# Kernel optimization log

Measured on AMD Instinct MI355X. Metric: run time of the kernel, lower is better.

The kernel has to match this reference:

```python
import jax, jax.numpy as jnp
import numpy as np

B, N, E, H = 2, 2048, 1024, 16
D = E // H  # head_dim = 64


def setup_inputs() -> dict:
    key = jax.random.key(0)
    ks = jax.random.split(key, 8)
    s = 1.0 / np.sqrt(D)
    return {
        "query": jax.random.normal(ks[0], (B, N, E), jnp.float32),
        "key": jax.random.normal(ks[1], (B, N, E), jnp.float32),
        "value": jax.random.normal(ks[2], (B, N, E), jnp.float32),
        "mask": jax.random.randint(ks[3], (B, N), 0, 2, jnp.int32),
        # per-head Linear weights, torch layout (out_features, in_features) stacked over heads
        "Wq": jax.random.uniform(ks[4], (H, D, D), jnp.float32, -s, s),
        "Wk": jax.random.uniform(ks[5], (H, D, D), jnp.float32, -s, s),
        "Wv": jax.random.uniform(ks[6], (H, D, D), jnp.float32, -s, s),
        "Wo": jax.random.uniform(ks[7], (E, E), jnp.float32, -1.0 / np.sqrt(E), 1.0 / np.sqrt(E)),
    }


def reference(query, key, value, mask, Wq, Wk, Wv, Wo):
    b, n, e = query.shape
    h, d, _ = Wq.shape
    q = query.reshape(b, n, h, d)
    k = key.reshape(b, n, h, d)
    v = value.reshape(b, n, h, d)
    # per-head Linear (no bias): x @ W[i].T, batched over heads
    qh = jnp.einsum('bnhd,hed->bnhe', q, Wq)
    kh = jnp.einsum('bnhd,hed->bnhe', k, Wk)
    vh = jnp.einsum('bnhd,hed->bnhe', v, Wv)
    # NOTE: original scales by sqrt(embed_size), not sqrt(head_dim)
    scores = jnp.einsum('bqhd,bkhd->bhqk', qh, kh) / (e ** 0.5)
    # NOTE: mask is unsqueezed on the KEY axis position in torch (dim=2),
    # so it masks entire QUERY rows, broadcasting over keys.
    scores = jnp.where(mask[:, None, :, None] == 0, jnp.float32(-1e28), scores)
    probs = jax.nn.softmax(scores, axis=-1)
    attn = jnp.einsum('bhqk,bkhd->bqhd', probs, vh).reshape(b, n, e)
    return attn @ Wo.T
```

## Files before the change

### kernel.cpp

```cpp
#include <hip/hip_runtime.h>
#include <hip/hip_bf16.h>

#define B_ 2
#define N_ 2048
#define E_ 1024
#define H_ 16
#define D_ 64
#define BH_ (B_ * H_)

typedef __attribute__((ext_vector_type(4))) float f32x4;
typedef __attribute__((ext_vector_type(8))) short bf16x8;
typedef __attribute__((ext_vector_type(4))) short s16x4;
typedef __attribute__((ext_vector_type(4))) int i32x4;

#define MFMA(a, b, c) __builtin_amdgcn_mfma_f32_16x16x32_bf16(a, b, c, 0, 0, 0)

static __device__ __forceinline__ unsigned short f2bf(float f) {
    unsigned int u = __builtin_bit_cast(unsigned int, f);
    u += 0x7fff + ((u >> 16) & 1);
    return (unsigned short)(u >> 16);
}
static __device__ __forceinline__ float bf2f(unsigned short s) {
    unsigned int u = ((unsigned int)s) << 16;
    return __builtin_bit_cast(float, u);
}
static __device__ __forceinline__ int pack2bf(float lo, float hi) {
    return (int)f2bf(lo) | ((int)f2bf(hi) << 16);
}
static __device__ __forceinline__ bf16x8 cvt8(const float* __restrict__ p) {
    f32x4 a = *(const f32x4*)p;
    f32x4 b = *(const f32x4*)(p + 4);
    bf16x8 r;
    r[0] = (short)f2bf(a.x); r[1] = (short)f2bf(a.y);
    r[2] = (short)f2bf(a.z); r[3] = (short)f2bf(a.w);
    r[4] = (short)f2bf(b.x); r[5] = (short)f2bf(b.y);
    r[6] = (short)f2bf(b.z); r[7] = (short)f2bf(b.w);
    return r;
}

__global__ __launch_bounds__(256, 4)
void proj_kernel(const float* __restrict__ q, const float* __restrict__ k,
                 const float* __restrict__ v,
                 const float* __restrict__ Wq, const float* __restrict__ Wk,
                 const float* __restrict__ Wv,
                 unsigned short* __restrict__ qh, unsigned short* __restrict__ kh,
                 unsigned short* __restrict__ vt) {
    const int z = blockIdx.z;
    const float* X = (z == 0) ? q : (z == 1) ? k : v;
    const float* W = (z == 0) ? Wq : (z == 1) ? Wk : Wv;
    unsigned short* out = (z == 0) ? qh : (z == 1) ? kh : vt;

    const int lane = threadIdx.x & 63;
    const int wave = threadIdx.x >> 6;
    const int l16  = lane & 15;
    const int quad = lane >> 4;
    const int bh = blockIdx.y;
    const int b = bh >> 4, h = bh & 15;
    const int n0 = blockIdx.x * 64;

    const int tok = n0 + wave * 16 + l16;
    const float* xrow = X + ((size_t)(b * N_ + tok)) * E_ + h * 64;
    bf16x8 xf[2];
    xf[0] = cvt8(xrow + quad * 8);
    xf[1] = cvt8(xrow + 32 + quad * 8);

    const float* Wh = W + (size_t)h * 64 * 64;
    bf16x8 wf[4][2];
#pragma unroll
    for (int t4 = 0; t4 < 4; ++t4) {
        const float* wrow = Wh + (t4 * 16 + l16) * 64;
        wf[t4][0] = cvt8(wrow + quad * 8);
        wf[t4][1] = cvt8(wrow + 32 + quad * 8);
    }

    if (z != 2) {
#pragma unroll
        for (int t4 = 0; t4 < 4; ++t4) {
            f32x4 a = {0.f, 0.f, 0.f, 0.f};
            a = MFMA(xf[0], wf[t4][0], a);
            a = MFMA(xf[1], wf[t4][1], a);
#pragma unroll
            for (int r = 0; r < 4; ++r) {
                int tk = n0 + wave * 16 + quad * 4 + r;
                out[((size_t)bh * N_ + tk) * 64 + t4 * 16 + l16] = (unsigned short)f2bf(a[r]);
            }
        }
    } else {
#pragma unroll
        for (int mi = 0; mi < 4; ++mi) {
            f32x4 a = {0.f, 0.f, 0.f, 0.f};
            a = MFMA(wf[mi][0], xf[0], a);
            a = MFMA(wf[mi][1], xf[1], a);
#pragma unroll
            for (int r = 0; r < 4; ++r) {
                int dout = mi * 16 + quad * 4 + r;
                out[((size_t)bh * 64 + dout) * N_ + (n0 + wave * 16 + l16)] =
                    (unsigned short)f2bf(a[r]);
            }
        }
    }
}

__global__ __launch_bounds__(256)
void cvt_wo_kernel(const float* __restrict__ wo, unsigned short* __restrict__ wob) {
    int idx = blockIdx.x * 256 + threadIdx.x;
    f32x4 v = *(const f32x4*)(wo + (size_t)idx * 4);
    s16x4 r = {(short)f2bf(v.x), (short)f2bf(v.y), (short)f2bf(v.z), (short)f2bf(v.w)};
    *(s16x4*)(wob + (size_t)idx * 4) = r;
}

__global__ __launch_bounds__(256, 2)
void attn_kernel(const unsigned short* __restrict__ qh,
                 const unsigned short* __restrict__ kh,
                 const unsigned short* __restrict__ vt,
                 const int* __restrict__ mask,
                 unsigned short* __restrict__ attnb) {
    __shared__ short Kb[2][64][72];
    __shared__ short Vb[2][64][72];

    const int tid  = threadIdx.x;
    const int lane = tid & 63;
    const int wave = tid >> 6;
    const int l16  = lane & 15;
    const int quad = lane >> 4;

    const int flat = blockIdx.y * gridDim.x + blockIdx.x;
    const int qblk = flat >> 5;
    const int rem  = flat & 31;
    const int bh   = ((rem & 7) << 2) | (rem >> 3);
    const int b = bh >> 4, h = bh & 15;
    const int q0 = qblk * 128 + wave * 32;

    const unsigned short* kbase = kh + (size_t)bh * N_ * 64;
    const unsigned short* vbase = vt + (size_t)bh * 64 * N_;

    const int c0i = tid;
    const int c1i = tid + 256;

    const int srcA = (((quad * 2) & 3) << 4) + l16;
    const int srcB = (((quad * 2 + 1) & 3) << 4) + l16;
    const bool hiSel = (quad >= 2);

    const float qscale = 1.44269504f * 0.03125f;
    bf16x8 qf[2][2];
#pragma unroll
    for (int qi = 0; qi < 2; ++qi) {
        const int qrow_idx = q0 + qi * 16 + l16;
        const int mk = mask[b * N_ + qrow_idx];
        const unsigned short* qrow = qh + ((size_t)bh * N_ + qrow_idx) * 64;
#pragma unroll
        for (int c = 0; c < 2; ++c) {
            bf16x8 raw = *(const bf16x8*)(qrow + c * 32 + quad * 8);
            bf16x8 t;
#pragma unroll
            for (int j = 0; j < 8; ++j) {
                float f = bf2f((unsigned short)raw[j]) * qscale;
                t[j] = mk ? (short)f2bf(f) : (short)0;
            }
            qf[qi][c] = t;
        }
    }

    float lI[2] = {0.f, 0.f};
    f32x4 o[4][2];
#pragma unroll
    for (int mi = 0; mi < 4; ++mi)
#pragma unroll
        for (int qi = 0; qi < 2; ++qi) o[mi][qi] = (f32x4){0.f, 0.f, 0.f, 0.f};

    bf16x8 gK0, gK1, gV0, gV1;
    gK0 = *(const bf16x8*)(kbase + c0i * 8);
    gK1 = *(const bf16x8*)(kbase + c1i * 8);
    gV0 = *(const bf16x8*)(vbase + (size_t)(c0i >> 3) * N_ + (c0i & 7) * 8);
    gV1 = *(const bf16x8*)(vbase + (size_t)(c1i >> 3) * N_ + (c1i & 7) * 8);
    *(bf16x8*)(&Kb[0][c0i >> 3][(c0i & 7) * 8]) = gK0;
    *(bf16x8*)(&Kb[0][c1i >> 3][(c1i & 7) * 8]) = gK1;
    *(bf16x8*)(&Vb[0][c0i >> 3][(c0i & 7) * 8]) = gV0;
    *(bf16x8*)(&Vb[0][c1i >> 3][(c1i & 7) * 8]) = gV1;
    __syncthreads();

    for (int kt = 0; kt < N_ / 64; ++kt) {
        const int cur = kt & 1;

        if (kt + 1 < N_ / 64) {
            const int k0n = (kt + 1) * 64;
            gK0 = *(const bf16x8*)(kbase + (size_t)k0n * 64 + c0i * 8);
            gK1 = *(const bf16x8*)(kbase + (size_t)k0n * 64 + c1i * 8);
            gV0 = *(const bf16x8*)(vbase + (size_t)(c0i >> 3) * N_ + k0n + (c0i & 7) * 8);
            gV1 = *(const bf16x8*)(vbase + (size_t)(c1i >> 3) * N_ + k0n + (c1i & 7) * 8);
        }

        bf16x8 ka[4][2];
#pragma unroll
        for (int t4 = 0; t4 < 4; ++t4) {
            ka[t4][0] = *(const bf16x8*)(&Kb[cur][t4 * 16 + l16][quad * 8]);
            ka[t4][1] = *(const bf16x8*)(&Kb[cur][t4 * 16 + l16][32 + quad * 8]);
        }

        f32x4 s[2][4];
#pragma unroll
        for (int qi = 0; qi < 2; ++qi)
#pragma unroll
            for (int t4 = 0; t4 < 4; ++t4) {
                f32x4 z = {0.f, 0.f, 0.f, 0.f};
                z = MFMA(ka[t4][0], qf[qi][0], z);
                z = MFMA(ka[t4][1], qf[qi][1], z);
                s[qi][t4] = z;
            }

        bf16x8 va[4][2];
#pragma unroll
        for (int mi = 0; mi < 4; ++mi) {
            va[mi][0] = *(const bf16x8*)(&Vb[cur][mi * 16 + l16][quad * 8]);
            va[mi][1] = *(const bf16x8*)(&Vb[cur][mi * 16 + l16][32 + quad * 8]);
        }

#pragma unroll
        for (int qi = 0; qi < 2; ++qi) {
            float rsum = 0.f;
            int pk[4][2];
#pragma unroll
            for (int t4 = 0; t4 < 4; ++t4) {
                f32x4 p;
#pragma unroll
                for (int r = 0; r < 4; ++r) {
                    p[r] = __builtin_amdgcn_exp2f(s[qi][t4][r]);
                    rsum += p[r];
                }
                pk[t4][0] = pack2bf(p.x, p.y);
                pk[t4][1] = pack2bf(p.z, p.w);
            }
            rsum += __shfl_xor(rsum, 16);
            rsum += __shfl_xor(rsum, 32);
            lI[qi] += rsum;

            i32x4 w0, w1;
#pragma unroll
            for (int d = 0; d < 2; ++d) {
                int a0 = __shfl(pk[0][d], srcA), a1 = __shfl(pk[1][d], srcA);
                int b0 = __shfl(pk[0][d], srcB), b1 = __shfl(pk[1][d], srcB);
                w0[d]     = hiSel ? a1 : a0;
                w0[2 + d] = hiSel ? b1 : b0;
                int c0 = __shfl(pk[2][d], srcA), c1 = __shfl(pk[3][d], srcA);
                int e0 = __shfl(pk[2][d], srcB), e1 = __shfl(pk[3][d], srcB);
                w1[d]     = hiSel ? c1 : c0;
                w1[2 + d] = hiSel ? e1 : e0;
            }
            bf16x8 pb0 = __builtin_bit_cast(bf16x8, w0);
            bf16x8 pb1 = __builtin_bit_cast(bf16x8, w1);

#pragma unroll
            for (int mi = 0; mi < 4; ++mi) {
                o[mi][qi] = MFMA(va[mi][0], pb0, o[mi][qi]);
                o[mi][qi] = MFMA(va[mi][1], pb1, o[mi][qi]);
            }
        }

        if (kt + 1 < N_ / 64) {
            const int nxt = cur ^ 1;
            *(bf16x8*)(&Kb[nxt][c0i >> 3][(c0i & 7) * 8]) = gK0;
            *(bf16x8*)(&Kb[nxt][c1i >> 3][(c1i & 7) * 8]) = gK1;
            *(bf16x8*)(&Vb[nxt][c0i >> 3][(c0i & 7) * 8]) = gV0;
            *(bf16x8*)(&Vb[nxt][c1i >> 3][(c1i & 7) * 8]) = gV1;
            __syncthreads();
        }
    }

#pragma unroll
    for (int qi = 0; qi < 2; ++qi) {
        const float inv = 1.0f / lI[qi];
        const int qrow_idx = q0 + qi * 16 + l16;
#pragma unroll
        for (int mi = 0; mi < 4; ++mi) {
            f32x4 ov = o[mi][qi];
            s16x4 pkk = {(short)f2bf(ov.x * inv), (short)f2bf(ov.y * inv),
                         (short)f2bf(ov.z * inv), (short)f2bf(ov.w * inv)};
            int d0 = mi * 16 + quad * 4;
            *(s16x4*)(attnb + ((size_t)(b * N_ + qrow_idx)) * E_ + h * 64 + d0) = pkk;
        }
    }
}

__global__ __launch_bounds__(256, 4)
void out_gemm_kernel(const unsigned short* __restrict__ attnb,
                     const unsigned short* __restrict__ wob,
                     float* __restrict__ out) {
    const int lane = threadIdx.x & 63;
    const int wave = threadIdx.x >> 6;
    const int l16  = lane & 15;
    const int quad = lane >> 4;

    const int flat = blockIdx.y * gridDim.x + blockIdx.x;
    const int t0b  = ((flat & 7) << 2) | ((flat >> 3) & 3);
    const int c0b  = flat >> 5;
    const int t0 = t0b * 128 + wave * 32;
    const int c0 = c0b * 64;

    f32x4 acc[2][4];
#pragma unroll
    for (int mi = 0; mi < 2; ++mi)
#pragma unroll
        for (int t4 = 0; t4 < 4; ++t4) acc[mi][t4] = (f32x4){0.f, 0.f, 0.f, 0.f};

#pragma unroll 2
    for (int kc = 0; kc < E_ / 32; ++kc) {
        bf16x8 a[2], bb[4];
#pragma unroll
        for (int mi = 0; mi < 2; ++mi)
            a[mi] = *(const bf16x8*)(attnb + (size_t)(t0 + mi * 16 + l16) * E_ +
                                     kc * 32 + quad * 8);
#pragma unroll
        for (int t4 = 0; t4 < 4; ++t4)
            bb[t4] = *(const bf16x8*)(wob + (size_t)(c0 + t4 * 16 + l16) * E_ +
                                      kc * 32 + quad * 8);
#pragma unroll
        for (int mi = 0; mi < 2; ++mi)
#pragma unroll
            for (int t4 = 0; t4 < 4; ++t4)
                acc[mi][t4] = MFMA(a[mi], bb[t4], acc[mi][t4]);
    }

#pragma unroll
    for (int mi = 0; mi < 2; ++mi)
#pragma unroll
        for (int t4 = 0; t4 < 4; ++t4)
#pragma unroll
            for (int r = 0; r < 4; ++r)
                out[(size_t)(t0 + mi * 16 + quad * 4 + r) * E_ + c0 + t4 * 16 + l16] =
                    acc[mi][t4][r];
}

extern "C" void kernel_launch(void* const* d_in, const int* in_sizes, int n_in,
                              void* d_out, int out_size, void* d_ws, size_t ws_size,
                              hipStream_t stream) {
    const float* q    = (const float*)d_in[0];
    const float* k    = (const float*)d_in[1];
    const float* v    = (const float*)d_in[2];
    const int*   mask = (const int*)d_in[3];
    const float* Wq   = (const float*)d_in[4];
    const float* Wk   = (const float*)d_in[5];
    const float* Wv   = (const float*)d_in[6];
    const float* Wo   = (const float*)d_in[7];
    float* out = (float*)d_out;

    char* ws = (char*)d_ws;
    unsigned short* qh    = (unsigned short*)(ws);
    unsigned short* kh    = (unsigned short*)(ws + (size_t)8 * 1024 * 1024);
    unsigned short* vt    = (unsigned short*)(ws + (size_t)16 * 1024 * 1024);
    unsigned short* attnb = (unsigned short*)(ws + (size_t)24 * 1024 * 1024);
    unsigned short* wob   = (unsigned short*)(ws);

    dim3 blk(256);
    proj_kernel<<<dim3(N_ / 64, BH_, 3), blk, 0, stream>>>(q, k, v, Wq, Wk, Wv, qh, kh, vt);
    attn_kernel<<<dim3(16, 32), blk, 0, stream>>>(qh, kh, vt, mask, attnb);
    cvt_wo_kernel<<<dim3(E_ * E_ / 1024), blk, 0, stream>>>(Wo, wob);
    out_gemm_kernel<<<dim3(32, 16), blk, 0, stream>>>(attnb, wob, out);
}
```

Measured before the change: 241.8 us.

## Fold Q scale and mask into projection; LDS-tiled out GEMM with async loads

Result: faster. 224.2 us (-7.3%).

```diff
diff --git a/kernel.cpp b/kernel.cpp
--- a/kernel.cpp
+++ b/kernel.cpp
@@ -15,6 +15,9 @@
 
 #define MFMA(a, b, c) __builtin_amdgcn_mfma_f32_16x16x32_bf16(a, b, c, 0, 0, 0)
 
+#define AS1(p) ((const __attribute__((address_space(1))) unsigned int*)(p))
+#define AS3(p) ((__attribute__((address_space(3))) unsigned int*)(p))
+
 static __device__ __forceinline__ unsigned short f2bf(float f) {
     unsigned int u = __builtin_bit_cast(unsigned int, f);
     u += 0x7fff + ((u >> 16) & 1);
@@ -27,14 +30,14 @@
 static __device__ __forceinline__ int pack2bf(float lo, float hi) {
     return (int)f2bf(lo) | ((int)f2bf(hi) << 16);
 }
-static __device__ __forceinline__ bf16x8 cvt8(const float* __restrict__ p) {
+static __device__ __forceinline__ bf16x8 cvt8s(const float* __restrict__ p, float sc) {
     f32x4 a = *(const f32x4*)p;
     f32x4 b = *(const f32x4*)(p + 4);
     bf16x8 r;
-    r[0] = (short)f2bf(a.x); r[1] = (short)f2bf(a.y);
-    r[2] = (short)f2bf(a.z); r[3] = (short)f2bf(a.w);
-    r[4] = (short)f2bf(b.x); r[5] = (short)f2bf(b.y);
-    r[6] = (short)f2bf(b.z); r[7] = (short)f2bf(b.w);
+    r[0] = (short)f2bf(a.x * sc); r[1] = (short)f2bf(a.y * sc);
+    r[2] = (short)f2bf(a.z * sc); r[3] = (short)f2bf(a.w * sc);
+    r[4] = (short)f2bf(b.x * sc); r[5] = (short)f2bf(b.y * sc);
+    r[6] = (short)f2bf(b.z * sc); r[7] = (short)f2bf(b.w * sc);
     return r;
 }
 
@@ -43,12 +46,14 @@
                  const float* __restrict__ v,
                  const float* __restrict__ Wq, const float* __restrict__ Wk,
                  const float* __restrict__ Wv,
+                 const int* __restrict__ mask,
                  unsigned short* __restrict__ qh, unsigned short* __restrict__ kh,
                  unsigned short* __restrict__ vt) {
     const int z = blockIdx.z;
     const float* X = (z == 0) ? q : (z == 1) ? k : v;
     const float* W = (z == 0) ? Wq : (z == 1) ? Wk : Wv;
     unsigned short* out = (z == 0) ? qh : (z == 1) ? kh : vt;
+    const float wscale = (z == 0) ? (1.44269504f * 0.03125f) : 1.0f;
 
     const int lane = threadIdx.x & 63;
     const int wave = threadIdx.x >> 6;
@@ -57,45 +62,39 @@
     const int bh = blockIdx.y;
     const int b = bh >> 4, h = bh & 15;
     const int n0 = blockIdx.x * 64;
-
     const int tok = n0 + wave * 16 + l16;
+
     const float* xrow = X + ((size_t)(b * N_ + tok)) * E_ + h * 64;
     bf16x8 xf[2];
-    xf[0] = cvt8(xrow + quad * 8);
-    xf[1] = cvt8(xrow + 32 + quad * 8);
+    xf[0] = cvt8s(xrow + quad * 8, 1.0f);
+    xf[1] = cvt8s(xrow + 32 + quad * 8, 1.0f);
 
     const float* Wh = W + (size_t)h * 64 * 64;
     bf16x8 wf[4][2];
 #pragma unroll
     for (int t4 = 0; t4 < 4; ++t4) {
         const float* wrow = Wh + (t4 * 16 + l16) * 64;
-        wf[t4][0] = cvt8(wrow + quad * 8);
-        wf[t4][1] = cvt8(wrow + 32 + quad * 8);
-    }
-
-    if (z != 2) {
-#pragma unroll
-        for (int t4 = 0; t4 < 4; ++t4) {
-            f32x4 a = {0.f, 0.f, 0.f, 0.f};
-            a = MFMA(xf[0], wf[t4][0], a);
-            a = MFMA(xf[1], wf[t4][1], a);
-#pragma unroll
-            for (int r = 0; r < 4; ++r) {
-                int tk = n0 + wave * 16 + quad * 4 + r;
-                out[((size_t)bh * N_ + tk) * 64 + t4 * 16 + l16] = (unsigned short)f2bf(a[r]);
-            }
-        }
-    } else {
-#pragma unroll
-        for (int mi = 0; mi < 4; ++mi) {
-            f32x4 a = {0.f, 0.f, 0.f, 0.f};
-            a = MFMA(wf[mi][0], xf[0], a);
-            a = MFMA(wf[mi][1], xf[1], a);
+        wf[t4][0] = cvt8s(wrow + quad * 8, wscale);
+        wf[t4][1] = cvt8s(wrow + 32 + quad * 8, wscale);
+    }
+
+    const int mk = (z == 0) ? mask[b * N_ + tok] : 1;
+
+#pragma unroll
+    for (int mi = 0; mi < 4; ++mi) {
+        f32x4 a = {0.f, 0.f, 0.f, 0.f};
+        a = MFMA(wf[mi][0], xf[0], a);
+        a = MFMA(wf[mi][1], xf[1], a);
+        if (z != 2) {
+            s16x4 pk = {(short)f2bf(a.x), (short)f2bf(a.y),
+                        (short)f2bf(a.z), (short)f2bf(a.w)};
+            if (!mk) pk = (s16x4){0, 0, 0, 0};
+            *(s16x4*)(out + ((size_t)bh * N_ + tok) * 64 + mi * 16 + quad * 4) = pk;
+        } else {
 #pragma unroll
             for (int r = 0; r < 4; ++r) {
                 int dout = mi * 16 + quad * 4 + r;
-                out[((size_t)bh * 64 + dout) * N_ + (n0 + wave * 16 + l16)] =
-                    (unsigned short)f2bf(a[r]);
+                out[((size_t)bh * 64 + dout) * N_ + tok] = (unsigned short)f2bf(a[r]);
             }
         }
     }
@@ -113,7 +112,6 @@
 void attn_kernel(const unsigned short* __restrict__ qh,
                  const unsigned short* __restrict__ kh,
                  const unsigned short* __restrict__ vt,
-                 const int* __restrict__ mask,
                  unsigned short* __restrict__ attnb) {
     __shared__ short Kb[2][64][72];
     __shared__ short Vb[2][64][72];
@@ -141,24 +139,12 @@
     const int srcB = (((quad * 2 + 1) & 3) << 4) + l16;
     const bool hiSel = (quad >= 2);
 
-    const float qscale = 1.44269504f * 0.03125f;
     bf16x8 qf[2][2];
 #pragma unroll
     for (int qi = 0; qi < 2; ++qi) {
-        const int qrow_idx = q0 + qi * 16 + l16;
-        const int mk = mask[b * N_ + qrow_idx];
-        const unsigned short* qrow = qh + ((size_t)bh * N_ + qrow_idx) * 64;
-#pragma unroll
-        for (int c = 0; c < 2; ++c) {
-            bf16x8 raw = *(const bf16x8*)(qrow + c * 32 + quad * 8);
-            bf16x8 t;
-#pragma unroll
-            for (int j = 0; j < 8; ++j) {
-                float f = bf2f((unsigned short)raw[j]) * qscale;
-                t[j] = mk ? (short)f2bf(f) : (short)0;
-            }
-            qf[qi][c] = t;
-        }
+        const unsigned short* qrow = qh + ((size_t)bh * N_ + q0 + qi * 16 + l16) * 64;
+        qf[qi][0] = *(const bf16x8*)(qrow + quad * 8);
+        qf[qi][1] = *(const bf16x8*)(qrow + 32 + quad * 8);
     }
 
     float lI[2] = {0.f, 0.f};
@@ -281,53 +267,80 @@
     }
 }
 
-__global__ __launch_bounds__(256, 4)
-void out_gemm_kernel(const unsigned short* __restrict__ attnb,
-                     const unsigned short* __restrict__ wob,
+__global__ __launch_bounds__(256, 2)
+void out_gemm_kernel(const unsigned short* __restrict__ A,
+                     const unsigned short* __restrict__ Bw,
                      float* __restrict__ out) {
-    const int lane = threadIdx.x & 63;
-    const int wave = threadIdx.x >> 6;
+    __shared__ short As[2][128 * 32];
+    __shared__ short Bs[2][128 * 32];
+
+    const int tid  = threadIdx.x;
+    const int lane = tid & 63;
+    const int wave = tid >> 6;
     const int l16  = lane & 15;
     const int quad = lane >> 4;
-
-    const int flat = blockIdx.y * gridDim.x + blockIdx.x;
-    const int t0b  = ((flat & 7) << 2) | ((flat >> 3) & 3);
-    const int c0b  = flat >> 5;
-    const int t0 = t0b * 128 + wave * 32;
-    const int c0 = c0b * 64;
-
-    f32x4 acc[2][4];
-#pragma unroll
-    for (int mi = 0; mi < 2; ++mi)
-#pragma unroll
-        for (int t4 = 0; t4 < 4; ++t4) acc[mi][t4] = (f32x4){0.f, 0.f, 0.f, 0.f};
-
-#pragma unroll 2
-    for (int kc = 0; kc < E_ / 32; ++kc) {
-        bf16x8 a[2], bb[4];
-#pragma unroll
-        for (int mi = 0; mi < 2; ++mi)
-            a[mi] = *(const bf16x8*)(attnb + (size_t)(t0 + mi * 16 + l16) * E_ +
-                                     kc * 32 + quad * 8);
-#pragma unroll
-        for (int t4 = 0; t4 < 4; ++t4)
-            bb[t4] = *(const bf16x8*)(wob + (size_t)(c0 + t4 * 16 + l16) * E_ +
-                                      kc * 32 + quad * 8);
-#pragma unroll
-        for (int mi = 0; mi < 2; ++mi)
-#pragma unroll
-            for (int t4 = 0; t4 < 4; ++t4)
-                acc[mi][t4] = MFMA(a[mi], bb[t4], acc[mi][t4]);
-    }
-
-#pragma unroll
-    for (int mi = 0; mi < 2; ++mi)
-#pragma unroll
-        for (int t4 = 0; t4 < 4; ++t4)
+    const int wm = wave & 1, wn = wave >> 1;
+    const int m0 = blockIdx.x * 128;
+    const int n0 = blockIdx.y * 128;
+
+    const unsigned short* gA = A + (size_t)m0 * E_;
+    const unsigned short* gB = Bw + (size_t)n0 * E_;
+
+    f32x4 acc[4][4];
+#pragma unroll
+    for (int mt = 0; mt < 4; ++mt)
+#pragma unroll
+        for (int nt = 0; nt < 4; ++nt) acc[mt][nt] = (f32x4){0.f, 0.f, 0.f, 0.f};
+
+#define OG_STAGE(buf, k0)                                                        \
+    {                                                                            \
+        _Pragma("unroll")                                                        \
+        for (int j = 0; j < 2; ++j) {                                            \
+            const int p = j * 256 + wave * 64 + lane;                            \
+            const int c = p >> 7, r = p & 127;                                   \
+            const int lb = (j * 256 + wave * 64) * 8;                            \
+            __builtin_amdgcn_global_load_lds(                                    \
+                AS1(gA + (size_t)r * E_ + (k0) + c * 8),                         \
+                AS3(&As[buf][lb]), 16, 0, 0);                                    \
+            __builtin_amdgcn_global_load_lds(                                    \
+                AS1(gB + (size_t)r * E_ + (k0) + c * 8),                         \
+                AS3(&Bs[buf][lb]), 16, 0, 0);                                    \
+        }                                                                        \
+    }
+
+    OG_STAGE(0, 0)
+    __syncthreads();
+
+    for (int kt = 0; kt < E_ / 32; ++kt) {
+        const int cur = kt & 1;
+        if (kt + 1 < E_ / 32) OG_STAGE(cur ^ 1, (kt + 1) * 32)
+
+        bf16x8 af[4], bf[4];
+#pragma unroll
+        for (int mt = 0; mt < 4; ++mt)
+            af[mt] = *(const bf16x8*)(&As[cur][(quad * 128 + wm * 64 + mt * 16 + l16) * 8]);
+#pragma unroll
+        for (int nt = 0; nt < 4; ++nt)
+            bf[nt] = *(const bf16x8*)(&Bs[cur][(quad * 128 + wn * 64 + nt * 16 + l16) * 8]);
+
+#pragma unroll
+        for (int mt = 0; mt < 4; ++mt)
+#pragma unroll
+            for (int nt = 0; nt < 4; ++nt)
+                acc[mt][nt] = MFMA(af[mt], bf[nt], acc[mt][nt]);
+
+        __syncthreads();
+    }
+
+#pragma unroll
+    for (int mt = 0; mt < 4; ++mt)
+#pragma unroll
+        for (int nt = 0; nt < 4; ++nt)
 #pragma unroll
             for (int r = 0; r < 4; ++r)
-                out[(size_t)(t0 + mi * 16 + quad * 4 + r) * E_ + c0 + t4 * 16 + l16] =
-                    acc[mi][t4][r];
+                out[(size_t)(m0 + wm * 64 + mt * 16 + quad * 4 + r) * E_ +
+                    n0 + wn * 64 + nt * 16 + l16] = acc[mt][nt][r];
+#undef OG_STAGE
 }
 
 extern "C" void kernel_launch(void* const* d_in, const int* in_sizes, int n_in,
@@ -351,8 +364,9 @@
     unsigned short* wob   = (unsigned short*)(ws);
 
     dim3 blk(256);
-    proj_kernel<<<dim3(N_ / 64, BH_, 3), blk, 0, stream>>>(q, k, v, Wq, Wk, Wv, qh, kh, vt);
-    attn_kernel<<<dim3(16, 32), blk, 0, stream>>>(qh, kh, vt, mask, attnb);
+    proj_kernel<<<dim3(N_ / 64, BH_, 3), blk, 0, stream>>>(q, k, v, Wq, Wk, Wv, mask,
+                                                           qh, kh, vt);
+    attn_kernel<<<dim3(16, 32), blk, 0, stream>>>(qh, kh, vt, attnb);
     cvt_wo_kernel<<<dim3(E_ * E_ / 1024), blk, 0, stream>>>(Wo, wob);
-    out_gemm_kernel<<<dim3(32, 16), blk, 0, stream>>>(attnb, wob, out);
-}
+    out_gemm_kernel<<<dim3(32, 8), blk, 0, stream>>>(attnb, wob, out);
+}
```
